# Optimization experiments

Hardware: AMD Instinct MI355X
Metric: run time of the kernel (lower is better)

The kernel has to match this reference:

```python
import jax, jax.numpy as jnp
import numpy as np

H = 8  # attention heads
L = 2  # transformer layers


def conv1d(x, w, b=None, pad=0, dil=1):
    # x: (B, Cin, T), w: (Cout, Cin, K)
    y = jax.lax.conv_general_dilated(x, w, window_strides=(1,), padding=[(pad, pad)],
                                     rhs_dilation=(dil,), dimension_numbers=('NCH', 'OIH', 'NCH'))
    if b is not None:
        y = y + b[None, :, None]
    return y


def bn1d(x, p, eps=1e-5):
    # eval-mode BatchNorm1d; p: (4, C) = [gamma, beta, running_mean, running_var]
    g, b, m, v = p
    return g[None, :, None] * (x - m[None, :, None]) * jax.lax.rsqrt(v + eps)[None, :, None] + b[None, :, None]


def layernorm(x, g, b, eps=1e-5):
    m = x.mean(-1, keepdims=True)
    v = ((x - m) ** 2).mean(-1, keepdims=True)
    return (x - m) * jax.lax.rsqrt(v + eps) * g + b


def mha(x, in_w, in_b, out_w, out_b):
    # x: (T, B, E) seq-first, like nn.MultiheadAttention (eval, no dropout)
    T, B, E = x.shape
    dh = E // H
    qkv = x @ in_w.T + in_b
    q, k, v = jnp.split(qkv, 3, axis=-1)
    sh = lambda a: a.reshape(T, B, H, dh).transpose(1, 2, 0, 3)  # (B, H, T, dh)
    q, k, v = sh(q), sh(k), sh(v)
    attn = jax.nn.softmax(jnp.einsum('bhqd,bhkd->bhqk', q, k) * (dh ** -0.5), axis=-1)
    o = jnp.einsum('bhqk,bhkd->bhqd', attn, v).transpose(2, 0, 1, 3).reshape(T, B, E)
    return o @ out_w.T + out_b


def _forward(x, wts, cw1, cb1, bn1, cw2, cb2, bn2, cw3, cb3, bn3, cw4, cb4, bn4, cw5,
             tcw_in, tcb_in, t_in_w, t_in_b, t_out_w, t_out_b, ln1_g, ln1_b,
             ff_w1, ff_b1, ff_w2, ff_b2, ln2_g, ln2_b, tcw_out, tcb_out,
             cw6, bn6, bw1, bb1, bw2, bb2, bw3, bb3):
    out = x.transpose(0, 2, 1)  # (B, 2048, T)
    residual = out
    # multi-dilation conv branches: Conv1d -> ReLU -> BN
    o1 = bn1d(jax.nn.relu(conv1d(out, cw1, cb1, pad=1)), bn1)
    o2 = bn1d(jax.nn.relu(conv1d(out, cw2, cb2, pad=2, dil=2)), bn2)
    o3 = bn1d(jax.nn.relu(conv1d(out, cw3, cb3, pad=4, dil=4)), bn3)
    o4 = bn1d(jax.nn.relu(conv1d(out, cw4, cb4, pad=8, dil=4)), bn4)  # k=5, d=4, p=8
    out_d = wts[0] * o1 + wts[1] * o2 + wts[2] * o3 + wts[3] * o4  # (B, 512, T)
    # conv_5: 2048 -> 512, k=1, no bias
    out = jax.nn.relu(conv1d(out, cw5))
    # TransformerFeatureAggregator
    out = conv1d(out, tcw_in, tcb_in)  # 1x1 conv 512->512
    out = out.transpose(2, 0, 1)  # (T, B, 512)
    for i in range(L):
        a = mha(out, t_in_w[i], t_in_b[i], t_out_w[i], t_out_b[i])
        out = layernorm(out + a, ln1_g[i], ln1_b[i])
        ff = jax.nn.relu(out @ ff_w1[i].T + ff_b1[i]) @ ff_w2[i].T + ff_b2[i]
        out = layernorm(out + ff, ln2_g[i], ln2_b[i])
    out = out.transpose(1, 2, 0)  # (B, 512, T)
    out = conv1d(out, tcw_out, tcb_out)
    out = jnp.concatenate([out_d, out], axis=1)  # (B, 1024, T)
    out = bn1d(jax.nn.relu(conv1d(out, cw6, pad=1)), bn6)  # (B, 2048, T)
    # Bottleneck residual block
    r = out
    b = jax.nn.relu(conv1d(out, bw1, bb1))
    b = jax.nn.relu(conv1d(b, bw2, bb2, pad=1))
    b = conv1d(b, bw3, bb3)
    out = jax.nn.relu(b + r)
    out = out + residual
    return out.transpose(0, 2, 1)  # (B, T, 2048)


def setup_inputs() -> dict:
    key = jax.random.key(0)
    ks = iter(jax.random.split(key, 80))

    def rn(shape, s=0.02):
        return jax.random.normal(next(ks), shape, jnp.float32) * s

    def bn_p(c):
        return jnp.stack([1.0 + rn((c,), 0.1), rn((c,), 0.1), rn((c,), 0.1),
                          0.5 + jax.random.uniform(next(ks), (c,), jnp.float32)])

    B, T, D = 8, 1024, 2048
    return dict(
        x=jax.random.normal(next(ks), (B, T, D), jnp.float32),
        wts=jnp.ones((4,), jnp.float32),
        cw1=rn((512, D, 3)), cb1=rn((512,)), bn1=bn_p(512),
        cw2=rn((512, D, 3)), cb2=rn((512,)), bn2=bn_p(512),
        cw3=rn((512, D, 3)), cb3=rn((512,)), bn3=bn_p(512),
        cw4=rn((512, D, 5)), cb4=rn((512,)), bn4=bn_p(512),
        cw5=rn((512, D, 1)),
        tcw_in=rn((512, 512, 1)), tcb_in=rn((512,)),
        t_in_w=rn((L, 3 * 512, 512)), t_in_b=rn((L, 3 * 512)),
        t_out_w=rn((L, 512, 512)), t_out_b=rn((L, 512)),
        ln1_g=jnp.ones((L, 512), jnp.float32), ln1_b=jnp.zeros((L, 512), jnp.float32),
        ff_w1=rn((L, 2048, 512)), ff_b1=rn((L, 2048)),
        ff_w2=rn((L, 512, 2048)), ff_b2=rn((L, 512)),
        ln2_g=jnp.ones((L, 512), jnp.float32), ln2_b=jnp.zeros((L, 512), jnp.float32),
        tcw_out=rn((512, 512, 1)), tcb_out=rn((512,)),
        cw6=rn((2048, 1024, 3)), bn6=bn_p(2048),
        bw1=rn((512, 2048, 1)), bb1=rn((512,)),
        bw2=rn((512, 512, 3)), bb2=rn((512,)),
        bw3=rn((2048, 512, 1)), bb3=rn((2048,)),
    )


def reference(x, wts, cw1, cb1, bn1, cw2, cb2, bn2, cw3, cb3, bn3, cw4, cb4, bn4, cw5,
              tcw_in, tcb_in, t_in_w, t_in_b, t_out_w, t_out_b, ln1_g, ln1_b,
              ff_w1, ff_b1, ff_w2, ff_b2, ln2_g, ln2_b, tcw_out, tcb_out,
              cw6, bn6, bw1, bb1, bw2, bb2, bw3, bb3):
    return _forward(x, wts, cw1, cb1, bn1, cw2, cb2, bn2, cw3, cb3, bn3, cw4, cb4, bn4, cw5,
                    tcw_in, tcb_in, t_in_w, t_in_b, t_out_w, t_out_b, ln1_g, ln1_b,
                    ff_w1, ff_b1, ff_w2, ff_b2, ln2_g, ln2_b, tcw_out, tcb_out,
                    cw6, bn6, bw1, bb1, bw2, bb2, bw3, bb3)
```

## Files before the change

### kernel.cpp

```cpp
#include <hip/hip_runtime.h>
#include <hip/hip_bf16.h>


typedef __attribute__((ext_vector_type(4))) float f32x4;
typedef __attribute__((ext_vector_type(8))) short short8;
typedef __attribute__((ext_vector_type(8))) unsigned short ushort8;

__device__ __forceinline__ unsigned short f2bu(float f) {
    __hip_bfloat16 h = __float2bfloat16(f);
    return *reinterpret_cast<unsigned short*>(&h);
}
__device__ __forceinline__ float bu2f(unsigned short u) {
    __hip_bfloat16 h = *reinterpret_cast<__hip_bfloat16*>(&u);
    return __bfloat162float(h);
}

__device__ __forceinline__ void gload16(const void* g, void* l) {
    __builtin_amdgcn_global_load_lds(
        (const __attribute__((address_space(1))) unsigned int*)g,
        (__attribute__((address_space(3))) unsigned int*)l, 16, 0, 0);
}

__global__ void cast_kernel(const float* __restrict__ in, unsigned short* __restrict__ out, int n8)
{
    for (int i = blockIdx.x * blockDim.x + threadIdx.x; i < n8; i += gridDim.x * blockDim.x) {
        const float4* p = (const float4*)in + (size_t)i * 2;
        float4 a = p[0], b = p[1];
        ushort8 o;
        o[0] = f2bu(a.x); o[1] = f2bu(a.y); o[2] = f2bu(a.z); o[3] = f2bu(a.w);
        o[4] = f2bu(b.x); o[5] = f2bu(b.y); o[6] = f2bu(b.z); o[7] = f2bu(b.w);
        *(ushort8*)(out + (size_t)i * 8) = o;
    }
}

struct WJob { const float* src; unsigned short* dst; int N, K, taps; };
struct WJobs { WJob j[14]; int n; };

__global__ void wtrans_multi(WJobs jobs)
{
    for (int q = 0; q < jobs.n; ++q) {
        const float* __restrict__ src = jobs.j[q].src;
        unsigned short* __restrict__ dst = jobs.j[q].dst;
        const int N = jobs.j[q].N, K = jobs.j[q].K, taps = jobs.j[q].taps;
        const int total = N * K * taps;
        for (int idx = blockIdx.x * blockDim.x + threadIdx.x; idx < total;
             idx += gridDim.x * blockDim.x) {
            int i   = idx % K;
            int rem = idx / K;
            int o   = rem % N;
            int k   = rem / N;
            dst[idx] = f2bu(src[((size_t)o * K + i) * (size_t)taps + k]);
        }
    }
}

template<int BM_, int EPI>
__global__ __launch_bounds__(256)
void mgemm(const __hip_bfloat16* __restrict__ A, int lda,
           const __hip_bfloat16* __restrict__ Bw, const float* __restrict__ bias,
           float* __restrict__ Cf, __hip_bfloat16* __restrict__ Cb, int ldc,
           int N, int K,
           const float* __restrict__ r1, int ldr, const float* __restrict__ r2)
{
    constexpr int MREP = BM_ / 32;
    __shared__ __align__(16) short As[2][BM_ * 32];
    __shared__ __align__(16) short Bs[2][128 * 32];

    const int tid  = threadIdx.x;
    const int w    = tid >> 6;
    const int lane = tid & 63;
    const int wr   = w >> 1, wc = w & 1;
    const int m_base = blockIdx.x * BM_;
    const int n_base = blockIdx.y * 128;
    const int lrr = lane >> 2;
    const int lj  = lane & 3;

    f32x4 acc[MREP][4];
#pragma unroll
    for (int m = 0; m < MREP; ++m)
#pragma unroll
        for (int n = 0; n < 4; ++n) acc[m][n] = (f32x4){0.f, 0.f, 0.f, 0.f};

    auto stage = [&](int nb, int kc) {
#pragma unroll
        for (int cb = 0; cb < 2; ++cb) {
            const int cc = w + cb * 4;
            const int r  = cc * 16 + lrr;
            const int jc = lj ^ (r & 3);
            gload16((const void*)(Bw + (size_t)(n_base + r) * K + kc + jc * 8),
                    (void*)&Bs[nb][cc * 512]);
        }
#pragma unroll
        for (int ca = 0; ca < BM_ / 64; ++ca) {
            const int cc = w + ca * 4;
            const int r  = cc * 16 + lrr;
            const int jc = lj ^ (r & 3);
            gload16((const void*)(A + (size_t)(m_base + r) * lda + kc + jc * 8),
                    (void*)&As[nb][cc * 512]);
        }
    };

    stage(0, 0);
    __syncthreads();
    int cur = 0;
    const int nt = K / 32;
    for (int t = 0; t < nt; ++t) {
        if (t + 1 < nt) stage(cur ^ 1, (t + 1) * 32);

        short8 a[MREP], b[4];
#pragma unroll
        for (int m = 0; m < MREP; ++m) {
            const int i = wr * (BM_ / 2) + m * 16 + (lane & 15);
            a[m] = *(const short8*)&As[cur][i * 32 + (((lane >> 4) ^ (i & 3)) * 8)];
        }
#pragma unroll
        for (int n = 0; n < 4; ++n) {
            const int r = wc * 64 + n * 16 + (lane & 15);
            b[n] = *(const short8*)&Bs[cur][r * 32 + (((lane >> 4) ^ (r & 3)) * 8)];
        }
#pragma unroll
        for (int m = 0; m < MREP; ++m)
#pragma unroll
            for (int n = 0; n < 4; ++n)
                acc[m][n] = __builtin_amdgcn_mfma_f32_16x16x32_bf16(a[m], b[n], acc[m][n], 0, 0, 0);

        __syncthreads();
        cur ^= 1;
    }

#pragma unroll
    for (int m = 0; m < MREP; ++m) {
#pragma unroll
        for (int n = 0; n < 4; ++n) {
#pragma unroll
            for (int j = 0; j < 4; ++j) {
                const int row = m_base + wr * (BM_ / 2) + m * 16 + (lane >> 4) * 4 + j;
                const int col = n_base + wc * 64 + n * 16 + (lane & 15);
                float v = acc[m][n][j];
                if (bias) v += bias[col];
                const size_t idx = (size_t)row * ldc + col;
                if (EPI == 1) v = fmaxf(v, 0.f);
                if (EPI == 3) {
                    v += r1[(size_t)row * ldr + col];
                    v = fmaxf(v, 0.f) + r2[(size_t)row * 2048 + col];
                    Cf[idx] = v;
                } else {
                    if (Cf) Cf[idx] = v;
                    if (Cb) Cb[idx] = __float2bfloat16(v);
                }
            }
        }
    }
}

template<int NTAPS, int EPI>
__global__ __launch_bounds__(256)
void cgemm(const __hip_bfloat16* __restrict__ A1, const __hip_bfloat16* __restrict__ A2,
           int split, int lda,
           const __hip_bfloat16* __restrict__ Bw, const float* __restrict__ bias,
           float* __restrict__ Cf, __hip_bfloat16* __restrict__ Cb, int ldc,
           int N, int K,
           int o0, int o1, int o2,
           const float* __restrict__ bnp,
           const __hip_bfloat16* __restrict__ zb)
{
    __shared__ __align__(16) short As[144 * 32];
    __shared__ __align__(16) short Bs[NTAPS * 128 * 32];

    const int tid  = threadIdx.x;
    const int w    = tid >> 6;
    const int lane = tid & 63;
    const int wr   = w >> 1, wc = w & 1;
    const int m_base = blockIdx.x * 128;
    const int n_base = blockIdx.y * 128;
    const int tb   = m_base & 1023;
    const int lrr  = lane >> 2;
    const int lj   = lane & 3;

    f32x4 acc[4][4];
#pragma unroll
    for (int m = 0; m < 4; ++m)
#pragma unroll
        for (int n = 0; n < 4; ++n) acc[m][n] = (f32x4){0.f, 0.f, 0.f, 0.f};

    for (int kc = 0; kc < K; kc += 32) {
        __syncthreads();
        for (int c = w; c < 9; c += 4) {
            const int i    = c * 16 + lrr;
            const int jc   = lj ^ (i & 3);
            const int trow = tb + i - 8;
            const int c0   = kc + jc * 8;
            const void* src;
            if ((unsigned)trow < 1024u) {
                const int g = m_base - 8 + i;
                src = (c0 < split) ? (const void*)(A1 + (size_t)g * lda + c0)
                                   : (const void*)(A2 + (size_t)g * lda + (c0 - split));
            } else {
                src = (const void*)(zb + jc * 8);
            }
            gload16(src, (void*)&As[c * 512]);
        }
        for (int cb = w; cb < NTAPS * 8; cb += 4) {
            const int tap = cb >> 3, sub = cb & 7;
            const int r   = sub * 16 + lrr;
            const int jc  = lj ^ (r & 3);
            gload16((const void*)(Bw + ((size_t)tap * N + n_base + r) * K + kc + jc * 8),
                    (void*)&Bs[cb * 512]);
        }
        __syncthreads();

#pragma unroll
        for (int tap = 0; tap < NTAPS; ++tap) {
            const int off = (tap == 0) ? o0 : (tap == 1) ? o1 : o2;
            short8 a[4], b[4];
#pragma unroll
            for (int m = 0; m < 4; ++m) {
                const int i = 8 + off + wr * 64 + m * 16 + (lane & 15);
                a[m] = *(const short8*)&As[i * 32 + (((lane >> 4) ^ (i & 3)) * 8)];
            }
#pragma unroll
            for (int n = 0; n < 4; ++n) {
                const int r = wc * 64 + n * 16 + (lane & 15);
                b[n] = *(const short8*)&Bs[tap * 4096 + r * 32 + (((lane >> 4) ^ (r & 3)) * 8)];
            }
#pragma unroll
            for (int m = 0; m < 4; ++m)
#pragma unroll
                for (int n = 0; n < 4; ++n)
                    acc[m][n] = __builtin_amdgcn_mfma_f32_16x16x32_bf16(a[m], b[n], acc[m][n], 0, 0, 0);
        }
    }

#pragma unroll
    for (int m = 0; m < 4; ++m) {
#pragma unroll
        for (int n = 0; n < 4; ++n) {
#pragma unroll
            for (int j = 0; j < 4; ++j) {
                const int row = m_base + wr * 64 + m * 16 + (lane >> 4) * 4 + j;
                const int col = n_base + wc * 64 + n * 16 + (lane & 15);
                float v = acc[m][n][j];
                if (bias) v += bias[col];
                const size_t idx = (size_t)row * ldc + col;
                if (EPI == 1) v = fmaxf(v, 0.f);
                if (EPI == 2) {
                    v = fmaxf(v, 0.f);
                    const float g  = bnp[col];
                    const float be = bnp[N + col];
                    const float mu = bnp[2 * N + col];
                    const float va = bnp[3 * N + col];
                    v = g * (v - mu) * rsqrtf(va + 1e-5f) + be;
                }
                if (Cf) Cf[idx] = v;
                if (Cb) Cb[idx] = __float2bfloat16(v);
            }
        }
    }
}

template<int NTAPS>
__global__ __launch_bounds__(256, 2)
void cgemm2(const __hip_bfloat16* __restrict__ A1, const __hip_bfloat16* __restrict__ A2,
            int split, int lda,
            const __hip_bfloat16* __restrict__ Bw, const float* __restrict__ bias,
            float* __restrict__ Cf, __hip_bfloat16* __restrict__ Cb, int ldc,
            int N, int K,
            int o0, int o1, int o2,
            const float* __restrict__ bnp,
            const __hip_bfloat16* __restrict__ zb)
{
    __shared__ __align__(16) short As[272 * 32];
    __shared__ __align__(16) short Bs[NTAPS * 128 * 32];

    const int tid  = threadIdx.x;
    const int w    = tid >> 6;
    const int lane = tid & 63;
    const int wr   = w >> 1, wc = w & 1;
    const int m_base = blockIdx.x * 256;
    const int n_base = blockIdx.y * 128;
    const int tb   = m_base & 1023;
    const int lrr  = lane >> 2;
    const int lj   = lane & 3;

    f32x4 acc[8][4];
#pragma unroll
    for (int m = 0; m < 8; ++m)
#pragma unroll
        for (int n = 0; n < 4; ++n) acc[m][n] = (f32x4){0.f, 0.f, 0.f, 0.f};

    for (int kc = 0; kc < K; kc += 32) {
        __syncthreads();
        for (int c = w; c < 17; c += 4) {
            const int i    = c * 16 + lrr;
            const int jc   = lj ^ (i & 3);
            const int trow = tb + i - 8;
            const int c0   = kc + jc * 8;
            const void* src;
            if ((unsigned)trow < 1024u) {
                const int g = m_base - 8 + i;
                src = (c0 < split) ? (const void*)(A1 + (size_t)g * lda + c0)
                                   : (const void*)(A2 + (size_t)g * lda + (c0 - split));
            } else {
                src = (const void*)(zb + jc * 8);
            }
            gload16(src, (void*)&As[c * 512]);
        }
        for (int cb = w; cb < NTAPS * 8; cb += 4) {
            const int tap = cb >> 3, sub = cb & 7;
            const int r   = sub * 16 + lrr;
            const int jc  = lj ^ (r & 3);
            gload16((const void*)(Bw + ((size_t)tap * N + n_base + r) * K + kc + jc * 8),
                    (void*)&Bs[cb * 512]);
        }
        __syncthreads();

#pragma unroll
        for (int tap = 0; tap < NTAPS; ++tap) {
            const int off = (tap == 0) ? o0 : (tap == 1) ? o1 : o2;
            short8 b[4];
#pragma unroll
            for (int n = 0; n < 4; ++n) {
                const int r = wc * 64 + n * 16 + (lane & 15);
                b[n] = *(const short8*)&Bs[tap * 4096 + r * 32 + (((lane >> 4) ^ (r & 3)) * 8)];
            }
#pragma unroll
            for (int m = 0; m < 8; ++m) {
                const int i = 8 + off + wr * 128 + m * 16 + (lane & 15);
                short8 a = *(const short8*)&As[i * 32 + (((lane >> 4) ^ (i & 3)) * 8)];
#pragma unroll
                for (int n = 0; n < 4; ++n)
                    acc[m][n] = __builtin_amdgcn_mfma_f32_16x16x32_bf16(a, b[n], acc[m][n], 0, 0, 0);
            }
        }
    }

#pragma unroll
    for (int m = 0; m < 8; ++m) {
#pragma unroll
        for (int n = 0; n < 4; ++n) {
#pragma unroll
            for (int j = 0; j < 4; ++j) {
                const int row = m_base + wr * 128 + m * 16 + (lane >> 4) * 4 + j;
                const int col = n_base + wc * 64 + n * 16 + (lane & 15);
                float v = acc[m][n][j];
                if (bias) v += bias[col];
                v = fmaxf(v, 0.f);
                const float g  = bnp[col];
                const float be = bnp[N + col];
                const float mu = bnp[2 * N + col];
                const float va = bnp[3 * N + col];
                v = g * (v - mu) * rsqrtf(va + 1e-5f) + be;
                const size_t idx = (size_t)row * ldc + col;
                if (Cf) Cf[idx] = v;
                if (Cb) Cb[idx] = __float2bfloat16(v);
            }
        }
    }
}

struct BrP {
    const __hip_bfloat16* W;
    const float* bias;
    const float* bn;
    __hip_bfloat16* out;
    int ntaps;
    int o0, o1, o2, o3, o4;
};
struct BrPs { BrP p[4]; };

__global__ __launch_bounds__(256, 2)
void bgemm(const __hip_bfloat16* __restrict__ A, BrPs ps,
           const float* __restrict__ wts,
           const __hip_bfloat16* __restrict__ zb)
{
    __shared__ __align__(16) short As[272 * 32];
    __shared__ __align__(16) short Bs[5 * 128 * 32];

    const int tid  = threadIdx.x;
    const int w    = tid >> 6;
    const int lane = tid & 63;
    const int wr   = w >> 1, wc = w & 1;
    const int m_base = blockIdx.x * 256;
    const int n_base = blockIdx.y * 128;
    const int z    = blockIdx.z;
    const BrP p    = ps.p[z];
    const int tb   = m_base & 1023;
    const int lrr  = lane >> 2;
    const int lj   = lane & 3;
    const int ntaps = p.ntaps;

    f32x4 acc[8][4];
#pragma unroll
    for (int m = 0; m < 8; ++m)
#pragma unroll
        for (int n = 0; n < 4; ++n) acc[m][n] = (f32x4){0.f, 0.f, 0.f, 0.f};

    for (int kc = 0; kc < 2048; kc += 32) {
        __syncthreads();
        for (int c = w; c < 17; c += 4) {
            const int i    = c * 16 + lrr;
            const int jc   = lj ^ (i & 3);
            const int trow = tb + i - 8;
            const void* src;
            if ((unsigned)trow < 1024u)
                src = (const void*)(A + (size_t)(m_base - 8 + i) * 2048 + kc + jc * 8);
            else
                src = (const void*)(zb + jc * 8);
            gload16(src, (void*)&As[c * 512]);
        }
        for (int cb = w; cb < ntaps * 8; cb += 4) {
            const int tap = cb >> 3, sub = cb & 7;
            const int r   = sub * 16 + lrr;
            const int jc  = lj ^ (r & 3);
            gload16((const void*)(p.W + ((size_t)tap * 512 + n_base + r) * 2048 + kc + jc * 8),
                    (void*)&Bs[cb * 512]);
        }
        __syncthreads();

#pragma unroll 5
        for (int tap = 0; tap < ntaps; ++tap) {
            const int off = (tap == 0) ? p.o0 : (tap == 1) ? p.o1 : (tap == 2) ? p.o2
                          : (tap == 3) ? p.o3 : p.o4;
            short8 b[4];
#pragma unroll
            for (int n = 0; n < 4; ++n) {
                const int r = wc * 64 + n * 16 + (lane & 15);
                b[n] = *(const short8*)&Bs[tap * 4096 + r * 32 + (((lane >> 4) ^ (r & 3)) * 8)];
            }
#pragma unroll
            for (int m = 0; m < 8; ++m) {
                const int i = 8 + off + wr * 128 + m * 16 + (lane & 15);
                short8 a = *(const short8*)&As[i * 32 + (((lane >> 4) ^ (i & 3)) * 8)];
#pragma unroll
                for (int n = 0; n < 4; ++n)
                    acc[m][n] = __builtin_amdgcn_mfma_f32_16x16x32_bf16(a, b[n], acc[m][n], 0, 0, 0);
            }
        }
    }

    const float wz = wts[z];
#pragma unroll
    for (int m = 0; m < 8; ++m) {
#pragma unroll
        for (int n = 0; n < 4; ++n) {
#pragma unroll
            for (int j = 0; j < 4; ++j) {
                const int row = m_base + wr * 128 + m * 16 + (lane >> 4) * 4 + j;
                const int col = n_base + wc * 64 + n * 16 + (lane & 15);
                float v = fmaxf(acc[m][n][j] + p.bias[col], 0.f);
                const float g  = p.bn[col];
                const float be = p.bn[512 + col];
                const float mu = p.bn[1024 + col];
                const float va = p.bn[1536 + col];
                v = (g * (v - mu) * rsqrtf(va + 1e-5f) + be) * wz;
                p.out[(size_t)row * 512 + col] = __float2bfloat16(v);
            }
        }
    }
}

__global__ void bsum_kernel(const unsigned short* __restrict__ b0, const unsigned short* __restrict__ b1,
                            const unsigned short* __restrict__ b2, const unsigned short* __restrict__ b3,
                            unsigned short* __restrict__ o, int n8)
{
    for (int i = blockIdx.x * blockDim.x + threadIdx.x; i < n8; i += gridDim.x * blockDim.x) {
        ushort8 v0 = *(const ushort8*)(b0 + (size_t)i * 8);
        ushort8 v1 = *(const ushort8*)(b1 + (size_t)i * 8);
        ushort8 v2 = *(const ushort8*)(b2 + (size_t)i * 8);
        ushort8 v3 = *(const ushort8*)(b3 + (size_t)i * 8);
        ushort8 r;
#pragma unroll
        for (int e = 0; e < 8; ++e)
            r[e] = f2bu(bu2f(v0[e]) + bu2f(v1[e]) + bu2f(v2[e]) + bu2f(v3[e]));
        *(ushort8*)(o + (size_t)i * 8) = r;
    }
}

__global__ __launch_bounds__(256)
void ln_kernel(float* __restrict__ x, const float* __restrict__ t,
               const float* __restrict__ g, const float* __restrict__ b,
               __hip_bfloat16* __restrict__ xb, int M)
{
    const int wave = threadIdx.x >> 6;
    const int lane = threadIdx.x & 63;
    const int row  = blockIdx.x * 4 + wave;
    if (row >= M) return;
    float* xr = x + (size_t)row * 512;
    const float* tr = t + (size_t)row * 512;
    float v[8];
    float s = 0.f, s2 = 0.f;
#pragma unroll
    for (int j = 0; j < 8; ++j) {
        float val = xr[lane * 8 + j] + tr[lane * 8 + j];
        v[j] = val; s += val; s2 += val * val;
    }
#pragma unroll
    for (int d = 1; d < 64; d <<= 1) {
        s  += __shfl_xor(s, d, 64);
        s2 += __shfl_xor(s2, d, 64);
    }
    const float mean = s * (1.f / 512.f);
    const float var  = s2 * (1.f / 512.f) - mean * mean;
    const float rstd = rsqrtf(var + 1e-5f);
#pragma unroll
    for (int j = 0; j < 8; ++j) {
        const int c = lane * 8 + j;
        const float o = (v[j] - mean) * rstd * g[c] + b[c];
        xr[c] = o;
        xb[(size_t)row * 512 + c] = __float2bfloat16(o);
    }
}

__global__ __launch_bounds__(256)
void mattn(const __hip_bfloat16* __restrict__ qkv, __hip_bfloat16* __restrict__ o)
{
    __shared__ __align__(16) short Ks[4096];
    __shared__ __align__(16) short Vt[4096];
    __shared__ __align__(16) short Pl[8192];

    const int tid  = threadIdx.x;
    const int w    = tid >> 6;
    const int lane = tid & 63;
    const int g    = lane >> 4;
    const int li   = lane & 15;
    const int b    = blockIdx.x >> 3;
    const int h    = blockIdx.x & 7;
    const int qb   = blockIdx.y * 128 + w * 32;

    const short* qkvs = (const short*)qkv;

    short8 qf[2][2];
#pragma unroll
    for (int m = 0; m < 2; ++m)
#pragma unroll
        for (int ks = 0; ks < 2; ++ks)
            qf[m][ks] = *(const short8*)(qkvs +
                (size_t)(b * 1024 + qb + m * 16 + li) * 1536 + h * 64 + ks * 32 + g * 8);

    f32x4 Oa[2][4];
    float mr[2][4], lr[2][4];
#pragma unroll
    for (int m = 0; m < 2; ++m)
#pragma unroll
        for (int j = 0; j < 4; ++j) { mr[m][j] = -1e30f; lr[m][j] = 0.f; }
#pragma unroll
    for (int m = 0; m < 2; ++m)
#pragma unroll
        for (int n = 0; n < 4; ++n) Oa[m][n] = (f32x4){0.f, 0.f, 0.f, 0.f};

    const int sr = tid >> 2;
    const int sc = (tid & 3) * 16;

    for (int kt = 0; kt < 16; ++kt) {
        __syncthreads();
        const short* kr = qkvs + (size_t)(b * 1024 + kt * 64 + sr) * 1536 + 512 + h * 64 + sc;
        short8 k0 = *(const short8*)kr;
        short8 k1 = *(const short8*)(kr + 8);
        short8 v0 = *(const short8*)(kr + 512);
        short8 v1 = *(const short8*)(kr + 520);
        const int swr = (sr & 7) << 4;
        *(short8*)&Ks[(sr * 128 + ((sc * 2) ^ swr)) >> 1] = k0;
        *(short8*)&Ks[(sr * 128 + ((sc * 2 + 16) ^ swr)) >> 1] = k1;
#pragma unroll
        for (int e = 0; e < 8; ++e) {
            const int d = sc + e;
            Vt[(d * 128 + ((sr * 2) ^ ((d & 7) << 4))) >> 1] = v0[e];
        }
#pragma unroll
        for (int e = 0; e < 8; ++e) {
            const int d = sc + 8 + e;
            Vt[(d * 128 + ((sr * 2) ^ ((d & 7) << 4))) >> 1] = v1[e];
        }
        __syncthreads();

        short8 kf[4][2], vf[4][2];
#pragma unroll
        for (int n = 0; n < 4; ++n) {
            const int r  = n * 16 + li;
            const int sw = (r & 7) << 4;
#pragma unroll
            for (int ks = 0; ks < 2; ++ks) {
                const int cb = ks * 64 + g * 16;
                kf[n][ks] = *(const short8*)&Ks[(r * 128 + (cb ^ sw)) >> 1];
                vf[n][ks] = *(const short8*)&Vt[(r * 128 + (cb ^ sw)) >> 1];
            }
        }

        f32x4 s[2][4];
#pragma unroll
        for (int m = 0; m < 2; ++m)
#pragma unroll
            for (int n = 0; n < 4; ++n) s[m][n] = (f32x4){0.f, 0.f, 0.f, 0.f};
#pragma unroll
        for (int m = 0; m < 2; ++m)
#pragma unroll
            for (int n = 0; n < 4; ++n)
#pragma unroll
                for (int ks = 0; ks < 2; ++ks)
                    s[m][n] = __builtin_amdgcn_mfma_f32_16x16x32_bf16(qf[m][ks], kf[n][ks], s[m][n], 0, 0, 0);

#pragma unroll
        for (int m = 0; m < 2; ++m) {
            float cc[4];
#pragma unroll
            for (int j = 0; j < 4; ++j) {
                float rm = fmaxf(fmaxf(s[m][0][j], s[m][1][j]), fmaxf(s[m][2][j], s[m][3][j]));
                rm *= 0.125f;
#pragma unroll
                for (int d = 1; d < 16; d <<= 1) rm = fmaxf(rm, __shfl_xor(rm, d, 64));
                const float mn = fmaxf(mr[m][j], rm);
                cc[j] = __expf(mr[m][j] - mn);
                mr[m][j] = mn;
            }
            float rs[4] = {0.f, 0.f, 0.f, 0.f};
#pragma unroll
            for (int n = 0; n < 4; ++n)
#pragma unroll
                for (int j = 0; j < 4; ++j) {
                    const float pv = __expf(s[m][n][j] * 0.125f - mr[m][j]);
                    rs[j] += pv;
                    const int r  = m * 16 + g * 4 + j;
                    const int cb = (n * 16 + li) * 2;
                    Pl[(w * 4096 + r * 128 + (cb ^ ((r & 7) << 4))) >> 1] = (short)f2bu(pv);
                }
#pragma unroll
            for (int j = 0; j < 4; ++j) {
#pragma unroll
                for (int d = 1; d < 16; d <<= 1) rs[j] += __shfl_xor(rs[j], d, 64);
                lr[m][j] = lr[m][j] * cc[j] + rs[j];
#pragma unroll
                for (int n = 0; n < 4; ++n) Oa[m][n][j] *= cc[j];
            }
        }
        __syncthreads();

        short8 pa[2][2];
#pragma unroll
        for (int m = 0; m < 2; ++m) {
            const int r  = m * 16 + li;
            const int sw = (r & 7) << 4;
#pragma unroll
            for (int ks = 0; ks < 2; ++ks) {
                const int cb = ks * 64 + g * 16;
                pa[m][ks] = *(const short8*)&Pl[(w * 4096 + r * 128 + (cb ^ sw)) >> 1];
            }
        }
#pragma unroll
        for (int m = 0; m < 2; ++m)
#pragma unroll
            for (int n = 0; n < 4; ++n)
#pragma unroll
                for (int ks = 0; ks < 2; ++ks)
                    Oa[m][n] = __builtin_amdgcn_mfma_f32_16x16x32_bf16(pa[m][ks], vf[n][ks], Oa[m][n], 0, 0, 0);
    }

#pragma unroll
    for (int m = 0; m < 2; ++m)
#pragma unroll
        for (int j = 0; j < 4; ++j) {
            const float inv = 1.f / lr[m][j];
            const size_t row = (size_t)(b * 1024 + qb + m * 16 + g * 4 + j);
#pragma unroll
            for (int n = 0; n < 4; ++n)
                o[row * 512 + h * 64 + n * 16 + li] = __float2bfloat16(Oa[m][n][j] * inv);
        }
}


extern "C" void kernel_launch(void* const* d_in, const int* in_sizes, int n_in,
                              void* d_out, int out_size, void* d_ws, size_t ws_size,
                              hipStream_t stream)
{
    const float* x       = (const float*)d_in[0];
    const float* wts     = (const float*)d_in[1];
    const float* cw1     = (const float*)d_in[2];
    const float* cb1     = (const float*)d_in[3];
    const float* bn1     = (const float*)d_in[4];
    const float* cw2     = (const float*)d_in[5];
    const float* cb2     = (const float*)d_in[6];
    const float* bn2     = (const float*)d_in[7];
    const float* cw3     = (const float*)d_in[8];
    const float* cb3     = (const float*)d_in[9];
    const float* bn3     = (const float*)d_in[10];
    const float* cw4     = (const float*)d_in[11];
    const float* cb4     = (const float*)d_in[12];
    const float* bn4     = (const float*)d_in[13];
    const float* cw5     = (const float*)d_in[14];
    const float* tcw_in  = (const float*)d_in[15];
    const float* tcb_in  = (const float*)d_in[16];
    const float* t_in_w  = (const float*)d_in[17];
    const float* t_in_b  = (const float*)d_in[18];
    const float* t_out_w = (const float*)d_in[19];
    const float* t_out_b = (const float*)d_in[20];
    const float* ln1_g   = (const float*)d_in[21];
    const float* ln1_b   = (const float*)d_in[22];
    const float* ff_w1   = (const float*)d_in[23];
    const float* ff_b1   = (const float*)d_in[24];
    const float* ff_w2   = (const float*)d_in[25];
    const float* ff_b2   = (const float*)d_in[26];
    const float* ln2_g   = (const float*)d_in[27];
    const float* ln2_b   = (const float*)d_in[28];
    const float* tcw_out = (const float*)d_in[29];
    const float* tcb_out = (const float*)d_in[30];
    const float* cw6     = (const float*)d_in[31];
    const float* bn6     = (const float*)d_in[32];
    const float* bw1     = (const float*)d_in[33];
    const float* bb1     = (const float*)d_in[34];
    const float* bw2     = (const float*)d_in[35];
    const float* bb2     = (const float*)d_in[36];
    const float* bw3     = (const float*)d_in[37];
    const float* bb3     = (const float*)d_in[38];
    float* out = (float*)d_out;

    const size_t HMB = 524288;
    char* ws = (char*)d_ws;
    auto BF = [&](double mb) { return (__hip_bfloat16*)(ws + (size_t)(mb * 2) * HMB); };
    auto FP = [&](double mb) { return (float*)(ws + (size_t)(mb * 2) * HMB); };

    __hip_bfloat16* xb    = BF(0);
    float*          h7    = FP(0);
    __hip_bfloat16* bigqb = BF(32);
    __hip_bfloat16* wc1   = BF(32);
    __hip_bfloat16* wc2   = BF(39);
    __hip_bfloat16* wc3   = BF(46);
    __hip_bfloat16* wc4   = BF(53);
    __hip_bfloat16* wc5   = BF(64);
    __hip_bfloat16* wti0  = BF(66.5);
    __hip_bfloat16* wti1  = BF(68);
    __hip_bfloat16* wto0  = BF(69.5);
    __hip_bfloat16* wto1  = BF(70);
    __hip_bfloat16* wf10  = BF(70.5);
    __hip_bfloat16* wf11  = BF(72.5);
    __hip_bfloat16* wf20  = BF(74.5);
    __hip_bfloat16* wf21  = BF(76.5);
    __hip_bfloat16* wtci  = BF(78.5);
    __hip_bfloat16* wtco  = BF(79);
    __hip_bfloat16* bigb  = BF(80);
    __hip_bfloat16* h7b   = BF(80);
    __hip_bfloat16* br0   = BF(112);
    __hip_bfloat16* br1   = BF(120);
    __hip_bfloat16* br2   = BF(128);
    __hip_bfloat16* br3   = BF(136);
    float*          tmp   = FP(112);
    float*          xtf   = FP(128);
    __hip_bfloat16* outdb = BF(144);
    __hip_bfloat16* wc6   = BF(152);
    __hip_bfloat16* wtb1  = BF(165);
    __hip_bfloat16* wtb2  = BF(167.5);
    __hip_bfloat16* wtb3  = BF(169);
    __hip_bfloat16* tmpb  = BF(171);
    __hip_bfloat16* atnb  = BF(171);
    __hip_bfloat16* xtfb  = BF(179);
    __hip_bfloat16* zb    = BF(188);

    const int M = 8192;
    dim3 blk(256);

    auto mg = [&](int bm, int epi, const __hip_bfloat16* A, int lda,
                  const __hip_bfloat16* Bw, const float* bias,
                  float* Cf, __hip_bfloat16* Cb, int ldc, int N, int K,
                  const float* r1, int ldr, const float* r2) {
        dim3 grid(M / bm, N / 128);
#define LAU(BMV, EPIV) mgemm<BMV, EPIV><<<grid, blk, 0, stream>>>(A, lda, Bw, bias, Cf, Cb, ldc, N, K, r1, ldr, r2)
        if (bm == 64) {
            switch (epi) { case 0: LAU(64, 0); break; case 1: LAU(64, 1); break;
                           default: LAU(64, 3); }
        } else {
            switch (epi) { case 0: LAU(128, 0); break; case 1: LAU(128, 1); break;
                           default: LAU(128, 3); }
        }
#undef LAU
    };

    hipMemsetAsync(zb, 0, 8192, stream);
    cast_kernel<<<dim3(2048), blk, 0, stream>>>(x, (unsigned short*)xb, M * 2048 / 8);

    WJobs early{};
    early.n = 5;
    early.j[0] = {cw1, (unsigned short*)wc1, 512, 2048, 3};
    early.j[1] = {cw2, (unsigned short*)wc2, 512, 2048, 3};
    early.j[2] = {cw3, (unsigned short*)wc3, 512, 2048, 3};
    early.j[3] = {cw4, (unsigned short*)wc4, 512, 2048, 5};
    early.j[4] = {cw5, (unsigned short*)wc5, 512, 2048, 1};
    wtrans_multi<<<dim3(2048), blk, 0, stream>>>(early);

    WJobs pers{};
    pers.n = 14;
    pers.j[0]  = {t_in_w,                (unsigned short*)wti0, 1536, 512, 1};
    pers.j[1]  = {t_in_w + 1536 * 512,   (unsigned short*)wti1, 1536, 512, 1};
    pers.j[2]  = {t_out_w,               (unsigned short*)wto0, 512, 512, 1};
    pers.j[3]  = {t_out_w + 512 * 512,   (unsigned short*)wto1, 512, 512, 1};
    pers.j[4]  = {ff_w1,                 (unsigned short*)wf10, 2048, 512, 1};
    pers.j[5]  = {ff_w1 + 2048 * 512,    (unsigned short*)wf11, 2048, 512, 1};
    pers.j[6]  = {ff_w2,                 (unsigned short*)wf20, 512, 2048, 1};
    pers.j[7]  = {ff_w2 + 512 * 2048,    (unsigned short*)wf21, 512, 2048, 1};
    pers.j[8]  = {tcw_in,                (unsigned short*)wtci, 512, 512, 1};
    pers.j[9]  = {tcw_out,               (unsigned short*)wtco, 512, 512, 1};
    pers.j[10] = {cw6,                   (unsigned short*)wc6, 2048, 1024, 3};
    pers.j[11] = {bw1,                   (unsigned short*)wtb1, 512, 2048, 1};
    pers.j[12] = {bw2,                   (unsigned short*)wtb2, 512, 512, 3};
    pers.j[13] = {bw3,                   (unsigned short*)wtb3, 2048, 512, 1};
    wtrans_multi<<<dim3(2048), blk, 0, stream>>>(pers);

    BrPs bp{};
    bp.p[0] = {wc1, cb1, bn1, br0, 3, -1, 0, 1, 0, 0};
    bp.p[1] = {wc2, cb2, bn2, br1, 3, -2, 0, 2, 0, 0};
    bp.p[2] = {wc3, cb3, bn3, br2, 3, -4, 0, 4, 0, 0};
    bp.p[3] = {wc4, cb4, bn4, br3, 5, -8, -4, 0, 4, 8};
    bgemm<<<dim3(M / 256, 4, 4), blk, 0, stream>>>(xb, bp, wts, zb);
    bsum_kernel<<<dim3(2048), blk, 0, stream>>>((const unsigned short*)br0, (const unsigned short*)br1,
                                                (const unsigned short*)br2, (const unsigned short*)br3,
                                                (unsigned short*)outdb, M * 512 / 8);

    mg(64, 1, xb, 2048, wc5, nullptr, nullptr, tmpb, 512, 512, 2048, nullptr, 0, nullptr);

    mg(64, 0, tmpb, 512, wtci, tcb_in, xtf, xtfb, 512, 512, 512, nullptr, 0, nullptr);

    for (int l = 0; l < 2; ++l) {
        const __hip_bfloat16* wi = l ? wti1 : wti0;
        const __hip_bfloat16* wo = l ? wto1 : wto0;
        const __hip_bfloat16* w1 = l ? wf11 : wf10;
        const __hip_bfloat16* w2 = l ? wf21 : wf20;
        mg(128, 0, xtfb, 512, wi, t_in_b + l * 1536, nullptr, bigqb, 1536, 1536, 512,
           nullptr, 0, nullptr);
        mattn<<<dim3(64, 8), blk, 0, stream>>>(bigqb, atnb);
        mg(64, 0, atnb, 512, wo, t_out_b + l * 512, tmp, nullptr, 512, 512, 512,
           nullptr, 0, nullptr);
        ln_kernel<<<dim3(M / 4), blk, 0, stream>>>(xtf, tmp, ln1_g + l * 512, ln1_b + l * 512, xtfb, M);
        mg(128, 1, xtfb, 512, w1, ff_b1 + l * 2048, nullptr, bigb, 2048, 2048, 512,
           nullptr, 0, nullptr);
        mg(64, 0, bigb, 2048, w2, ff_b2 + l * 512, tmp, nullptr, 512, 512, 2048,
           nullptr, 0, nullptr);
        ln_kernel<<<dim3(M / 4), blk, 0, stream>>>(xtf, tmp, ln2_g + l * 512, ln2_b + l * 512, xtfb, M);
    }

    mg(64, 0, xtfb, 512, wtco, tcb_out, nullptr, atnb, 512, 512, 512, nullptr, 0, nullptr);

    cgemm2<3><<<dim3(M / 256, 16), blk, 0, stream>>>(outdb, atnb, 512, 512, wc6, nullptr,
        h7, h7b, 2048, 2048, 1024, -1, 0, 1, bn6, zb);

    mg(64, 1, h7b, 2048, wtb1, bb1, nullptr, outdb, 512, 512, 2048, nullptr, 0, nullptr);
    cgemm<3, 1><<<dim3(M / 128, 4), blk, 0, stream>>>(outdb, outdb, 4096, 512, wtb2, bb2,
        nullptr, tmpb, 512, 512, 512, -1, 0, 1, nullptr, zb);
    mg(128, 3, tmpb, 512, wtb3, bb3, out, nullptr, 2048, 2048, 512, h7, 2048, x);

    (void)in_sizes; (void)n_in; (void)out_size; (void)ws_size;
}
```

Before: 1.254 ms.

## Fold conv5 GEMM into branch GEMM launch and change LDS swizzle key

Adds conv_5 (1x1, 2048->512, ReLU, no bias) as a fifth z-slice of the batched branch-conv kernel, so it shares one launch and the same input tiles instead of running as a separate GEMM. The epilogue now skips bias and BN when their pointers are null. Separately, the LDS XOR swizzle key changes from r&3 to (r>>2)&3 in every GEMM, which alters the bank-conflict pattern of the 16-byte LDS reads. The fused path runs on the bgemm 256x128 tile shape, whose efficiency for this N=512 slice may differ from the old 64-row mgemm.

```diff
diff --git a/kernel.cpp b/kernel.cpp
--- a/kernel.cpp
+++ b/kernel.cpp
@@ -54,6 +54,8 @@
     }
 }
 
+#define SKEY(r) (((r) >> 2) & 3)
+
 template<int BM_, int EPI>
 __global__ __launch_bounds__(256)
 void mgemm(const __hip_bfloat16* __restrict__ A, int lda,
@@ -86,7 +88,7 @@
         for (int cb = 0; cb < 2; ++cb) {
             const int cc = w + cb * 4;
             const int r  = cc * 16 + lrr;
-            const int jc = lj ^ (r & 3);
+            const int jc = lj ^ SKEY(r);
             gload16((const void*)(Bw + (size_t)(n_base + r) * K + kc + jc * 8),
                     (void*)&Bs[nb][cc * 512]);
         }
@@ -94,7 +96,7 @@
         for (int ca = 0; ca < BM_ / 64; ++ca) {
             const int cc = w + ca * 4;
             const int r  = cc * 16 + lrr;
-            const int jc = lj ^ (r & 3);
+            const int jc = lj ^ SKEY(r);
             gload16((const void*)(A + (size_t)(m_base + r) * lda + kc + jc * 8),
                     (void*)&As[nb][cc * 512]);
         }
@@ -111,12 +113,12 @@
 #pragma unroll
         for (int m = 0; m < MREP; ++m) {
             const int i = wr * (BM_ / 2) + m * 16 + (lane & 15);
-            a[m] = *(const short8*)&As[cur][i * 32 + (((lane >> 4) ^ (i & 3)) * 8)];
+            a[m] = *(const short8*)&As[cur][i * 32 + (((lane >> 4) ^ SKEY(i)) * 8)];
         }
 #pragma unroll
         for (int n = 0; n < 4; ++n) {
             const int r = wc * 64 + n * 16 + (lane & 15);
-            b[n] = *(const short8*)&Bs[cur][r * 32 + (((lane >> 4) ^ (r & 3)) * 8)];
+            b[n] = *(const short8*)&Bs[cur][r * 32 + (((lane >> 4) ^ SKEY(r)) * 8)];
         }
 #pragma unroll
         for (int m = 0; m < MREP; ++m)
@@ -187,7 +189,7 @@
         __syncthreads();
         for (int c = w; c < 9; c += 4) {
             const int i    = c * 16 + lrr;
-            const int jc   = lj ^ (i & 3);
+            const int jc   = lj ^ SKEY(i);
             const int trow = tb + i - 8;
             const int c0   = kc + jc * 8;
             const void* src;
@@ -203,7 +205,7 @@
         for (int cb = w; cb < NTAPS * 8; cb += 4) {
             const int tap = cb >> 3, sub = cb & 7;
             const int r   = sub * 16 + lrr;
-            const int jc  = lj ^ (r & 3);
+            const int jc  = lj ^ SKEY(r);
             gload16((const void*)(Bw + ((size_t)tap * N + n_base + r) * K + kc + jc * 8),
                     (void*)&Bs[cb * 512]);
         }
@@ -216,12 +218,12 @@
 #pragma unroll
             for (int m = 0; m < 4; ++m) {
                 const int i = 8 + off + wr * 64 + m * 16 + (lane & 15);
-                a[m] = *(const short8*)&As[i * 32 + (((lane >> 4) ^ (i & 3)) * 8)];
+                a[m] = *(const short8*)&As[i * 32 + (((lane >> 4) ^ SKEY(i)) * 8)];
             }
 #pragma unroll
             for (int n = 0; n < 4; ++n) {
                 const int r = wc * 64 + n * 16 + (lane & 15);
-                b[n] = *(const short8*)&Bs[tap * 4096 + r * 32 + (((lane >> 4) ^ (r & 3)) * 8)];
+                b[n] = *(const short8*)&Bs[tap * 4096 + r * 32 + (((lane >> 4) ^ SKEY(r)) * 8)];
             }
 #pragma unroll
             for (int m = 0; m < 4; ++m)
@@ -292,7 +294,7 @@
         __syncthreads();
         for (int c = w; c < 17; c += 4) {
             const int i    = c * 16 + lrr;
-            const int jc   = lj ^ (i & 3);
+            const int jc   = lj ^ SKEY(i);
             const int trow = tb + i - 8;
             const int c0   = kc + jc * 8;
             const void* src;
@@ -308,7 +310,7 @@
         for (int cb = w; cb < NTAPS * 8; cb += 4) {
             const int tap = cb >> 3, sub = cb & 7;
             const int r   = sub * 16 + lrr;
-            const int jc  = lj ^ (r & 3);
+            const int jc  = lj ^ SKEY(r);
             gload16((const void*)(Bw + ((size_t)tap * N + n_base + r) * K + kc + jc * 8),
                     (void*)&Bs[cb * 512]);
         }
@@ -321,12 +323,12 @@
 #pragma unroll
             for (int n = 0; n < 4; ++n) {
                 const int r = wc * 64 + n * 16 + (lane & 15);
-                b[n] = *(const short8*)&Bs[tap * 4096 + r * 32 + (((lane >> 4) ^ (r & 3)) * 8)];
+                b[n] = *(const short8*)&Bs[tap * 4096 + r * 32 + (((lane >> 4) ^ SKEY(r)) * 8)];
             }
 #pragma unroll
             for (int m = 0; m < 8; ++m) {
                 const int i = 8 + off + wr * 128 + m * 16 + (lane & 15);
-                short8 a = *(const short8*)&As[i * 32 + (((lane >> 4) ^ (i & 3)) * 8)];
+                short8 a = *(const short8*)&As[i * 32 + (((lane >> 4) ^ SKEY(i)) * 8)];
 #pragma unroll
                 for (int n = 0; n < 4; ++n)
                     acc[m][n] = __builtin_amdgcn_mfma_f32_16x16x32_bf16(a, b[n], acc[m][n], 0, 0, 0);
@@ -366,7 +368,7 @@
     int ntaps;
     int o0, o1, o2, o3, o4;
 };
-struct BrPs { BrP p[4]; };
+struct BrPs { BrP p[5]; };
 
 __global__ __launch_bounds__(256, 2)
 void bgemm(const __hip_bfloat16* __restrict__ A, BrPs ps,
@@ -399,7 +401,7 @@
         __syncthreads();
         for (int c = w; c < 17; c += 4) {
             const int i    = c * 16 + lrr;
-            const int jc   = lj ^ (i & 3);
+            const int jc   = lj ^ SKEY(i);
             const int trow = tb + i - 8;
             const void* src;
             if ((unsigned)trow < 1024u)
@@ -411,7 +413,7 @@
         for (int cb = w; cb < ntaps * 8; cb += 4) {
             const int tap = cb >> 3, sub = cb & 7;
             const int r   = sub * 16 + lrr;
-            const int jc  = lj ^ (r & 3);
+            const int jc  = lj ^ SKEY(r);
             gload16((const void*)(p.W + ((size_t)tap * 512 + n_base + r) * 2048 + kc + jc * 8),
                     (void*)&Bs[cb * 512]);
         }
@@ -425,12 +427,12 @@
 #pragma unroll
             for (int n = 0; n < 4; ++n) {
                 const int r = wc * 64 + n * 16 + (lane & 15);
-                b[n] = *(const short8*)&Bs[tap * 4096 + r * 32 + (((lane >> 4) ^ (r & 3)) * 8)];
+                b[n] = *(const short8*)&Bs[tap * 4096 + r * 32 + (((lane >> 4) ^ SKEY(r)) * 8)];
             }
 #pragma unroll
             for (int m = 0; m < 8; ++m) {
                 const int i = 8 + off + wr * 128 + m * 16 + (lane & 15);
-                short8 a = *(const short8*)&As[i * 32 + (((lane >> 4) ^ (i & 3)) * 8)];
+                short8 a = *(const short8*)&As[i * 32 + (((lane >> 4) ^ SKEY(i)) * 8)];
 #pragma unroll
                 for (int n = 0; n < 4; ++n)
                     acc[m][n] = __builtin_amdgcn_mfma_f32_16x16x32_bf16(a, b[n], acc[m][n], 0, 0, 0);
@@ -438,7 +440,7 @@
         }
     }
 
-    const float wz = wts[z];
+    const float wz = wts[z & 3];
 #pragma unroll
     for (int m = 0; m < 8; ++m) {
 #pragma unroll
@@ -447,12 +449,16 @@
             for (int j = 0; j < 4; ++j) {
                 const int row = m_base + wr * 128 + m * 16 + (lane >> 4) * 4 + j;
                 const int col = n_base + wc * 64 + n * 16 + (lane & 15);
-                float v = fmaxf(acc[m][n][j] + p.bias[col], 0.f);
-                const float g  = p.bn[col];
-                const float be = p.bn[512 + col];
-                const float mu = p.bn[1024 + col];
-                const float va = p.bn[1536 + col];
-                v = (g * (v - mu) * rsqrtf(va + 1e-5f) + be) * wz;
+                float v = acc[m][n][j];
+                if (p.bias) v += p.bias[col];
+                v = fmaxf(v, 0.f);
+                if (p.bn) {
+                    const float g  = p.bn[col];
+                    const float be = p.bn[512 + col];
+                    const float mu = p.bn[1024 + col];
+                    const float va = p.bn[1536 + col];
+                    v = (g * (v - mu) * rsqrtf(va + 1e-5f) + be) * wz;
+                }
                 p.out[(size_t)row * 512 + col] = __float2bfloat16(v);
             }
         }
@@ -807,12 +813,11 @@
     bp.p[1] = {wc2, cb2, bn2, br1, 3, -2, 0, 2, 0, 0};
     bp.p[2] = {wc3, cb3, bn3, br2, 3, -4, 0, 4, 0, 0};
     bp.p[3] = {wc4, cb4, bn4, br3, 5, -8, -4, 0, 4, 8};
-    bgemm<<<dim3(M / 256, 4, 4), blk, 0, stream>>>(xb, bp, wts, zb);
+    bp.p[4] = {wc5, nullptr, nullptr, tmpb, 1, 0, 0, 0, 0, 0};
+    bgemm<<<dim3(M / 256, 4, 5), blk, 0, stream>>>(xb, bp, wts, zb);
     bsum_kernel<<<dim3(2048), blk, 0, stream>>>((const unsigned short*)br0, (const unsigned short*)br1,
                                                 (const unsigned short*)br2, (const unsigned short*)br3,
                                                 (unsigned short*)outdb, M * 512 / 8);
-
-    mg(64, 1, xb, 2048, wc5, nullptr, nullptr, tmpb, 512, 512, 2048, nullptr, 0, nullptr);
 
     mg(64, 0, tmpb, 512, wtci, tcb_in, xtf, xtfb, 512, 512, 512, nullptr, 0, nullptr);
 
```

New measurement: 1.240 ms. Within noise of the previous version (-1.1%).
